# Kernel tuning notes

Measured on AMD Instinct MI355X. Metric: run time of the kernel, lower is better.

The kernel has to match this reference:

```python
import jax, jax.numpy as jnp
import numpy as np

IGNORE_T = 0.6
L_NOOBJ = 0.5
L_PRIOR = 0.01
L_COORD = 5.0
L_OBJ = 1.0
L_CLS = 1.0
PRIOR_EPOCHS = 12
EPS = 1e-8


def _iou_xyxy(a, b):
    # a, b: (..., 4) broadcastable xyxy boxes -> (...,) IoU
    ix1 = jnp.maximum(a[..., 0], b[..., 0])
    iy1 = jnp.maximum(a[..., 1], b[..., 1])
    ix2 = jnp.minimum(a[..., 2], b[..., 2])
    iy2 = jnp.minimum(a[..., 3], b[..., 3])
    inter = jnp.clip(ix2 - ix1, 0.0) * jnp.clip(iy2 - iy1, 0.0)
    area_a = jnp.clip(a[..., 2] - a[..., 0], 0.0) * jnp.clip(a[..., 3] - a[..., 1], 0.0)
    area_b = jnp.clip(b[..., 2] - b[..., 0], 0.0) * jnp.clip(b[..., 3] - b[..., 1], 0.0)
    return inter / (area_a + area_b - inter + EPS)


def setup_inputs() -> dict:
    key = jax.random.key(0)
    k1, k2, k3 = jax.random.split(key, 3)
    bs, G, A, C = 16, 19, 5, 20
    pred_tensor = jax.random.normal(k1, (bs, G, G, A, 5 + C), dtype=jnp.float32)
    gt_tensor = jax.random.uniform(k2, (bs, G, G, A, 5 + C), dtype=jnp.float32)
    anchors = jax.random.uniform(k3, (A, 2), dtype=jnp.float32)  # anchors_rel in (0,1)
    return {"pred_tensor": pred_tensor, "gt_tensor": gt_tensor, "anchors": anchors, "epoch": 5}


def reference(pred_tensor, gt_tensor, anchors, epoch):
    bs, G, _, A, _ = pred_tensor.shape
    f32 = pred_tensor.dtype
    px, py, pw, ph = (pred_tensor[..., i] for i in range(4))  # each [bs,G,G,A]
    po = pred_tensor[..., 4]
    pcls = pred_tensor[..., 5:]
    gx, gy, gw, gh = (gt_tensor[..., i] for i in range(4))
    go = gt_tensor[..., 4]
    gcls = gt_tensor[..., 5:]

    aw = anchors[:, 0].reshape(1, 1, 1, A)
    ah = anchors[:, 1].reshape(1, 1, 1, A)

    # YOLOv2 parameterization
    pbx, pby = jax.nn.sigmoid(px), jax.nn.sigmoid(py)
    pbw, pbh = jnp.exp(pw) * aw, jnp.exp(ph) * ah
    gbw, gbh = jnp.exp(gw) * aw, jnp.exp(gh) * ah

    ii = jnp.arange(G, dtype=f32).reshape(1, G, 1, 1)  # row index (y offset)
    jj = jnp.arange(G, dtype=f32).reshape(1, 1, G, 1)  # col index (x offset)

    def xywh2xyxy(x, y, w, h):
        cx, cy = x + jj, y + ii
        cw, ch = w * G, h * G
        return jnp.stack([cx - cw / 2, cy - ch / 2, cx + cw / 2, cy + ch / 2], axis=-1)

    pred_box = xywh2xyxy(pbx, pby, pbw, pbh)  # [bs,G,G,A,4]
    gt_box = xywh2xyxy(gx, gy, gbw, gbh)      # [bs,G,G,A,4]

    # part 1: max IoU of each prediction vs all positive gts (densified, masked)
    N = G * G * A
    pf = pred_box.reshape(bs, N, 4)
    gf = gt_box.reshape(bs, N, 4)
    gmask = (go > 0.5).reshape(bs, N).astype(f32)
    iou = _iou_xyxy(pf[:, :, None, :], gf[:, None, :, :])  # [bs,N,N]
    # IoU >= 0, so multiplying by the mask and taking max matches the torch
    # per-image nonzero-gather loop (and yields 0 when an image has no gt).
    max_iou = jnp.max(iou * gmask[:, None, :], axis=2).reshape(bs, G, G, A)

    noobj_mask = ((go <= 0.5) & (max_iou < IGNORE_T)).astype(f32)
    pconf = jax.nn.sigmoid(po)
    loss_noobj = L_NOOBJ * noobj_mask * pconf ** 2

    # part 2: prior (anchor-fitting) loss for early epochs
    pred_xywh = pred_tensor[..., 0:4]
    if epoch < PRIOR_EPOCHS:
        loss_prior = (L_PRIOR * pred_xywh ** 2).sum()
    else:
        loss_prior = jnp.zeros((), dtype=f32)

    # part 3: positive-sample losses
    pos = (go > 0.5).astype(f32)  # [bs,G,G,A]
    fitt_xywh = jnp.stack([jax.nn.sigmoid(px), jax.nn.sigmoid(py), pw, ph], axis=-1)
    gt_xywh = gt_tensor[..., 0:4]
    loss_xywh = L_COORD * pos[..., None] * (gt_xywh - fitt_xywh) ** 2

    conf_iou = _iou_xyxy(pred_box, gt_box)  # [bs,G,G,A]
    loss_conf = L_OBJ * pos * (conf_iou - jax.lax.stop_gradient(pconf)) ** 2

    pprob = jax.nn.softmax(pcls, axis=-1)
    loss_cls = L_CLS * pos[..., None] * (gcls - pprob) ** 2

    total = (loss_noobj.sum() + loss_prior + loss_xywh.sum()
             + loss_conf.sum() + loss_cls.sum()) / bs
    return total
```

## Files before the change

### kernel.cpp

```cpp
#include <hip/hip_runtime.h>

#define G_ 19
#define A_ 5
#define C_ 20
#define BS_ 16
#define N_ (G_*G_*A_)
#define CHK 8
#define SEG 256
#define NBLK (BS_*CHK)
#define EPSF 1e-8f

#define OFF_P1  0
#define OFF_CP  (OFF_P1 + NBLK*4)
#define OFF_CN  (OFF_CP + NBLK*4)
#define OFF_PLB (OFF_CN + NBLK*4 + 4)
#define OFF_PLA (OFF_PLB + NBLK*SEG*16)
#define OFF_NLB (OFF_PLA + NBLK*SEG*4)
#define OFF_NLV (OFF_NLB + NBLK*SEG*16)
#define OFF_FLG (OFF_NLV + NBLK*SEG*4)

__device__ __forceinline__ float sigmoidf_(float x) {
    return 1.0f / (1.0f + __expf(-x));
}

__global__ __launch_bounds__(256) void k1_elemwise(
    const float* __restrict__ pred, const float* __restrict__ gt,
    const float* __restrict__ anch, const int* __restrict__ epoch_p,
    char* __restrict__ ws, float* __restrict__ out)
{
    float*    partial1 = (float*)(ws + OFF_P1);
    unsigned* cntP  = (unsigned*)(ws + OFF_CP);
    unsigned* cntN  = (unsigned*)(ws + OFF_CN);
    float4*   plbox = (float4*)(ws + OFF_PLB);
    float*    plab  = (float*) (ws + OFF_PLA);
    float4*   nlbox = (float4*)(ws + OFF_NLB);
    float*    nlval = (float*) (ws + OFF_NLV);
    unsigned* flags = (unsigned*)(ws + OFF_FLG);

    __shared__ __align__(16) float sp[256*25];
    __shared__ __align__(16) float sg[256*25];
    __shared__ float red[4];
    __shared__ int wpo[4], wno[4];

    const int tid  = threadIdx.x;
    const int lane = tid & 63, wid = tid >> 6;
    const int b    = blockIdx.y;
    const int ch   = blockIdx.x;
    const int blin = b * CHK + ch;

    flags[blin*SEG + tid] = 0u;
    if (blin == 0 && tid == 0) out[0] = 0.f;

    int n0   = ch * 256;
    int rows = min(256, N_ - n0);
    int ndw  = rows * 25;
    const float* srcP = pred + ((size_t)b*N_ + n0)*25;
    const float* srcG = gt   + ((size_t)b*N_ + n0)*25;
    for (int d = tid; d < ndw; d += 256) { sp[d] = srcP[d]; sg[d] = srcG[d]; }
    __syncthreads();

    int n = n0 + tid;
    bool valid = tid < rows;
    const float* P = sp + tid*25;
    const float* T = sg + tid*25;
    float local = 0.f;

    bool pos = false;
    float gx1=0, gy1=0, gx2=0, gy2=0, area_g=0;
    float px1=0, py1=0, px2=0, py2=0, pconf=0;

    if (valid) {
        int a  = n % A_;
        int g2 = (n / A_) % G_;
        int g1 = n / (A_ * G_);
        float px = P[0], py = P[1], pw = P[2], ph = P[3], po = P[4];
        float gx = T[0], gy = T[1], gw = T[2], gh = T[3], go = T[4];
        float aw = anch[a*2+0], ah = anch[a*2+1];

        float sx  = sigmoidf_(px), sy = sigmoidf_(py);
        float pbw = __expf(pw) * aw, pbh = __expf(ph) * ah;
        float gbw = __expf(gw) * aw, gbh = __expf(gh) * ah;

        float cxp = sx + (float)g2, cyp = sy + (float)g1;
        float hwp = pbw * (0.5f * G_), hhp = pbh * (0.5f * G_);
        px1 = cxp - hwp; py1 = cyp - hhp; px2 = cxp + hwp; py2 = cyp + hhp;

        float cxg = gx + (float)g2, cyg = gy + (float)g1;
        float hwg = gbw * (0.5f * G_), hhg = gbh * (0.5f * G_);
        gx1 = cxg - hwg; gy1 = cyg - hhg; gx2 = cxg + hwg; gy2 = cyg + hhg;

        pconf = sigmoidf_(po);
        float area_p = fmaxf(px2 - px1, 0.f) * fmaxf(py2 - py1, 0.f);
        area_g = fmaxf(gx2 - gx1, 0.f) * fmaxf(gy2 - gy1, 0.f);

        if (*epoch_p < 12) {
            local += 0.01f * (px*px + py*py + pw*pw + ph*ph);
        }
        pos = go > 0.5f;
        if (pos) {
            float d0 = gx - sx, d1 = gy - sy, d2 = gw - pw, d3 = gh - ph;
            local += 5.0f * (d0*d0 + d1*d1 + d2*d2 + d3*d3);
            float ix1 = fmaxf(px1, gx1), iy1 = fmaxf(py1, gy1);
            float ix2 = fminf(px2, gx2), iy2 = fminf(py2, gy2);
            float iw = fmaxf(ix2 - ix1, 0.f), ih = fmaxf(iy2 - iy1, 0.f);
            float inter = iw * ih;
            float iou = inter / (area_p + area_g - inter + EPSF);
            float dc = iou - pconf;
            local += dc * dc;
            float cl[C_];
            float m = -1e30f;
            #pragma unroll
            for (int c = 0; c < C_; c++) { cl[c] = P[5+c]; m = fmaxf(m, cl[c]); }
            float s = 0.f;
            #pragma unroll
            for (int c = 0; c < C_; c++) { cl[c] = __expf(cl[c] - m); s += cl[c]; }
            float inv = 1.0f / s;
            float acc = 0.f;
            #pragma unroll
            for (int c = 0; c < C_; c++) { float d = T[5+c] - cl[c]*inv; acc += d*d; }
            local += acc;
        }
        local *= (1.0f / BS_);
    }

    bool isPos = valid && pos;
    bool isNeg = valid && !pos;
    unsigned long long mp = __ballot(isPos);
    unsigned long long mn = __ballot(isNeg);
    unsigned long long ltm = (1ull << lane) - 1ull;
    int ppre = __popcll(mp & ltm);
    int npre = __popcll(mn & ltm);
    if (lane == 0) { wpo[wid] = __popcll(mp); wno[wid] = __popcll(mn); }
    __syncthreads();
    int pexc = 0, nexc = 0, tp = 0, tn = 0;
    #pragma unroll
    for (int w = 0; w < 4; w++) {
        if (w < wid) { pexc += wpo[w]; nexc += wno[w]; }
        tp += wpo[w]; tn += wno[w];
    }
    if (isPos) {
        int k = blin*SEG + pexc + ppre;
        plbox[k] = make_float4(gx1, gy1, gx2, gy2);
        plab[k]  = area_g;
    } else if (isNeg) {
        int k = blin*SEG + nexc + npre;
        nlbox[k] = make_float4(px1, py1, px2, py2);
        nlval[k] = (0.5f / BS_) * pconf * pconf;
    }
    if (tid == 0) { cntP[blin] = (unsigned)tp; cntN[blin] = (unsigned)tn; }

    for (int off = 32; off; off >>= 1) local += __shfl_down(local, off);
    if (lane == 0) red[wid] = local;
    __syncthreads();
    if (tid == 0) partial1[blin] = red[0] + red[1] + red[2] + red[3];
}

__global__ __launch_bounds__(256) void k2_pairmax(char* __restrict__ ws)
{
    const unsigned* cntP  = (const unsigned*)(ws + OFF_CP);
    const unsigned* cntN  = (const unsigned*)(ws + OFF_CN);
    const float4*   plbox = (const float4*)(ws + OFF_PLB);
    const float*    plab  = (const float*) (ws + OFF_PLA);
    const float4*   nlbox = (const float4*)(ws + OFF_NLB);
    unsigned*       flags = (unsigned*)(ws + OFF_FLG);

    const int jc = blockIdx.x;
    const int ip = blockIdx.y;
    const int b  = blockIdx.z;
    const int tid = threadIdx.x;

    const int jblin = b*CHK + jc;
    const int iblin0 = b*CHK + ip*2;
    const int iblin1 = iblin0 + 1;

    int jlen = (int)cntP[jblin];
    if (jlen <= 0) return;

    __shared__ float4 sbox[SEG];
    __shared__ float  sb06[SEG];
    if (tid < jlen) {
        sbox[tid] = plbox[jblin*SEG + tid];
        sb06[tid] = -0.6f * plab[jblin*SEG + tid];
    }
    __syncthreads();

    int n0 = (int)cntN[iblin0], n1 = (int)cntN[iblin1];
    bool v0 = tid < n0, v1 = tid < n1;
    float4 p0 = v0 ? nlbox[iblin0*SEG + tid] : make_float4(0,0,0,0);
    float4 p1 = v1 ? nlbox[iblin1*SEG + tid] : make_float4(0,0,0,0);
    float c0 = (p0.z - p0.x) * (p0.w - p0.y) + EPSF;
    float c1 = (p1.z - p1.x) * (p1.w - p1.y) + EPSF;

    float md0 = -1e30f, md1 = -1e30f;
    for (int j = 0; j < jlen; j++) {
        float4 g = sbox[j];
        float tt = sb06[j];
        float ax0 = fmaxf(p0.x, g.x), ay0 = fmaxf(p0.y, g.y);
        float bx0 = fminf(p0.z, g.z), by0 = fminf(p0.w, g.w);
        float in0 = fmaxf(bx0 - ax0, 0.f) * fmaxf(by0 - ay0, 0.f);
        md0 = fmaxf(md0, fmaf(1.6f, in0, tt));
        float ax1 = fmaxf(p1.x, g.x), ay1 = fmaxf(p1.y, g.y);
        float bx1 = fminf(p1.z, g.z), by1 = fminf(p1.w, g.w);
        float in1 = fmaxf(bx1 - ax1, 0.f) * fmaxf(by1 - ay1, 0.f);
        md1 = fmaxf(md1, fmaf(1.6f, in1, tt));
    }
    if (v0 && md0 >= 0.6f * c0) flags[iblin0*SEG + tid] = 1u;
    if (v1 && md1 >= 0.6f * c1) flags[iblin1*SEG + tid] = 1u;
}

__global__ __launch_bounds__(256) void k3_final(char* __restrict__ ws,
                                                float* __restrict__ out)
{
    const float*    partial1 = (const float*)(ws + OFF_P1);
    const unsigned* cntN  = (const unsigned*)(ws + OFF_CN);
    const float*    nlval = (const float*) (ws + OFF_NLV);
    const unsigned* flags = (const unsigned*)(ws + OFF_FLG);

    const int tid  = threadIdx.x;
    const int blin = blockIdx.x;
    const int lane = tid & 63, wid = tid >> 6;

    float v = 0.f;
    if (tid < (int)cntN[blin] && flags[blin*SEG + tid] == 0u)
        v = nlval[blin*SEG + tid];
    if (tid == 0) v += partial1[blin];

    for (int off = 32; off; off >>= 1) v += __shfl_down(v, off);
    __shared__ float red[4];
    if (lane == 0) red[wid] = v;
    __syncthreads();
    if (tid == 0) atomicAdd(out, red[0] + red[1] + red[2] + red[3]);
}

extern "C" void kernel_launch(void* const* d_in, const int* in_sizes, int n_in,
                              void* d_out, int out_size, void* d_ws, size_t ws_size,
                              hipStream_t stream) {
    const float* pred  = (const float*)d_in[0];
    const float* gt_   = (const float*)d_in[1];
    const float* anch  = (const float*)d_in[2];
    const int*   epoch = (const int*)d_in[3];
    float* out = (float*)d_out;
    char*  ws  = (char*)d_ws;

    dim3 g1(CHK, BS_);
    k1_elemwise<<<g1, 256, 0, stream>>>(pred, gt_, anch, epoch, ws, out);
    dim3 g2(CHK, CHK/2, BS_);
    k2_pairmax<<<g2, 256, 0, stream>>>(ws);
    k3_final<<<NBLK, 256, 0, stream>>>(ws, out);
}
```

Before: 28.50 us.

## Fuse pair-max and final reduction via per-image ticket and bitmask

Merges the pairwise max-IoU kernel and the final reduction kernel into one launch. Per-image ignore flags become 64-bit ballot masks combined with atomicOr, and the last-arriving block for each image, found through an atomic ticket counter, performs the masked sum of the no-object terms. The load of full chunks into shared memory is unrolled, and the -0.6 area scaling moves into the first kernel. This removes one kernel launch and the flag array traffic, at the cost of atomics, thread fences and a serialized tail reduction per image.

```diff
diff --git a/kernel.cpp b/kernel.cpp
--- a/kernel.cpp
+++ b/kernel.cpp
@@ -13,11 +13,12 @@
 #define OFF_P1  0
 #define OFF_CP  (OFF_P1 + NBLK*4)
 #define OFF_CN  (OFF_CP + NBLK*4)
-#define OFF_PLB (OFF_CN + NBLK*4 + 4)
+#define OFF_TK  (OFF_CN + NBLK*4)
+#define OFF_MSK (OFF_TK + 64)
+#define OFF_PLB (OFF_MSK + BS_*32*8)
 #define OFF_PLA (OFF_PLB + NBLK*SEG*16)
 #define OFF_NLB (OFF_PLA + NBLK*SEG*4)
 #define OFF_NLV (OFF_NLB + NBLK*SEG*16)
-#define OFF_FLG (OFF_NLV + NBLK*SEG*4)
 
 __device__ __forceinline__ float sigmoidf_(float x) {
     return 1.0f / (1.0f + __expf(-x));
@@ -31,11 +32,12 @@
     float*    partial1 = (float*)(ws + OFF_P1);
     unsigned* cntP  = (unsigned*)(ws + OFF_CP);
     unsigned* cntN  = (unsigned*)(ws + OFF_CN);
+    unsigned* ticket = (unsigned*)(ws + OFF_TK);
+    unsigned long long* mask = (unsigned long long*)(ws + OFF_MSK);
     float4*   plbox = (float4*)(ws + OFF_PLB);
     float*    plab  = (float*) (ws + OFF_PLA);
     float4*   nlbox = (float4*)(ws + OFF_NLB);
     float*    nlval = (float*) (ws + OFF_NLV);
-    unsigned* flags = (unsigned*)(ws + OFF_FLG);
 
     __shared__ __align__(16) float sp[256*25];
     __shared__ __align__(16) float sg[256*25];
@@ -48,15 +50,23 @@
     const int ch   = blockIdx.x;
     const int blin = b * CHK + ch;
 
-    flags[blin*SEG + tid] = 0u;
+    if (tid < 4)               mask[blin*4 + tid] = 0ull;
+    if (ch == 0 && tid == 0)   ticket[b] = 0u;
     if (blin == 0 && tid == 0) out[0] = 0.f;
 
     int n0   = ch * 256;
     int rows = min(256, N_ - n0);
-    int ndw  = rows * 25;
     const float* srcP = pred + ((size_t)b*N_ + n0)*25;
     const float* srcG = gt   + ((size_t)b*N_ + n0)*25;
-    for (int d = tid; d < ndw; d += 256) { sp[d] = srcP[d]; sg[d] = srcG[d]; }
+    if (rows == 256) {
+        #pragma unroll
+        for (int k = 0; k < 25; k++) sp[tid + k*256] = srcP[tid + k*256];
+        #pragma unroll
+        for (int k = 0; k < 25; k++) sg[tid + k*256] = srcG[tid + k*256];
+    } else {
+        int ndw = rows * 25;
+        for (int d = tid; d < ndw; d += 256) { sp[d] = srcP[d]; sg[d] = srcG[d]; }
+    }
     __syncthreads();
 
     int n = n0 + tid;
@@ -141,7 +151,7 @@
     if (isPos) {
         int k = blin*SEG + pexc + ppre;
         plbox[k] = make_float4(gx1, gy1, gx2, gy2);
-        plab[k]  = area_g;
+        plab[k]  = -0.6f * area_g;
     } else if (isNeg) {
         int k = blin*SEG + nexc + npre;
         nlbox[k] = make_float4(px1, py1, px2, py2);
@@ -155,78 +165,96 @@
     if (tid == 0) partial1[blin] = red[0] + red[1] + red[2] + red[3];
 }
 
-__global__ __launch_bounds__(256) void k2_pairmax(char* __restrict__ ws)
+__global__ __launch_bounds__(256) void k2_fused(char* __restrict__ ws,
+                                                float* __restrict__ out)
 {
+    const float*    partial1 = (const float*)(ws + OFF_P1);
     const unsigned* cntP  = (const unsigned*)(ws + OFF_CP);
     const unsigned* cntN  = (const unsigned*)(ws + OFF_CN);
+    unsigned*       ticket = (unsigned*)(ws + OFF_TK);
+    unsigned long long* mask = (unsigned long long*)(ws + OFF_MSK);
     const float4*   plbox = (const float4*)(ws + OFF_PLB);
     const float*    plab  = (const float*) (ws + OFF_PLA);
     const float4*   nlbox = (const float4*)(ws + OFF_NLB);
-    unsigned*       flags = (unsigned*)(ws + OFF_FLG);
-
+    const float*    nlval = (const float*) (ws + OFF_NLV);
+
+    const int tid = threadIdx.x;
+    const int lane = tid & 63, wid = tid >> 6;
     const int jc = blockIdx.x;
     const int ip = blockIdx.y;
     const int b  = blockIdx.z;
-    const int tid = threadIdx.x;
-
-    const int jblin = b*CHK + jc;
+
+    const int jblin  = b*CHK + jc;
     const int iblin0 = b*CHK + ip*2;
     const int iblin1 = iblin0 + 1;
 
-    int jlen = (int)cntP[jblin];
-    if (jlen <= 0) return;
-
     __shared__ float4 sbox[SEG];
     __shared__ float  sb06[SEG];
+    __shared__ int    sFin;
+    __shared__ unsigned long long smask[32];
+    __shared__ float  red[4];
+
+    const int jlen = (int)cntP[jblin];
     if (tid < jlen) {
         sbox[tid] = plbox[jblin*SEG + tid];
-        sb06[tid] = -0.6f * plab[jblin*SEG + tid];
-    }
-    __syncthreads();
-
-    int n0 = (int)cntN[iblin0], n1 = (int)cntN[iblin1];
-    bool v0 = tid < n0, v1 = tid < n1;
-    float4 p0 = v0 ? nlbox[iblin0*SEG + tid] : make_float4(0,0,0,0);
-    float4 p1 = v1 ? nlbox[iblin1*SEG + tid] : make_float4(0,0,0,0);
-    float c0 = (p0.z - p0.x) * (p0.w - p0.y) + EPSF;
-    float c1 = (p1.z - p1.x) * (p1.w - p1.y) + EPSF;
-
-    float md0 = -1e30f, md1 = -1e30f;
-    for (int j = 0; j < jlen; j++) {
-        float4 g = sbox[j];
-        float tt = sb06[j];
-        float ax0 = fmaxf(p0.x, g.x), ay0 = fmaxf(p0.y, g.y);
-        float bx0 = fminf(p0.z, g.z), by0 = fminf(p0.w, g.w);
-        float in0 = fmaxf(bx0 - ax0, 0.f) * fmaxf(by0 - ay0, 0.f);
-        md0 = fmaxf(md0, fmaf(1.6f, in0, tt));
-        float ax1 = fmaxf(p1.x, g.x), ay1 = fmaxf(p1.y, g.y);
-        float bx1 = fminf(p1.z, g.z), by1 = fminf(p1.w, g.w);
-        float in1 = fmaxf(bx1 - ax1, 0.f) * fmaxf(by1 - ay1, 0.f);
-        md1 = fmaxf(md1, fmaf(1.6f, in1, tt));
-    }
-    if (v0 && md0 >= 0.6f * c0) flags[iblin0*SEG + tid] = 1u;
-    if (v1 && md1 >= 0.6f * c1) flags[iblin1*SEG + tid] = 1u;
-}
-
-__global__ __launch_bounds__(256) void k3_final(char* __restrict__ ws,
-                                                float* __restrict__ out)
-{
-    const float*    partial1 = (const float*)(ws + OFF_P1);
-    const unsigned* cntN  = (const unsigned*)(ws + OFF_CN);
-    const float*    nlval = (const float*) (ws + OFF_NLV);
-    const unsigned* flags = (const unsigned*)(ws + OFF_FLG);
-
-    const int tid  = threadIdx.x;
-    const int blin = blockIdx.x;
-    const int lane = tid & 63, wid = tid >> 6;
+        sb06[tid] = plab [jblin*SEG + tid];
+    }
+    __syncthreads();
+
+    if (jlen > 0) {
+        int n0 = (int)cntN[iblin0], n1 = (int)cntN[iblin1];
+        bool v0 = tid < n0, v1 = tid < n1;
+        float4 p0 = nlbox[iblin0*SEG + tid];
+        float4 p1 = nlbox[iblin1*SEG + tid];
+        float t00 = 0.6f * ((p0.z - p0.x) * (p0.w - p0.y) + EPSF);
+        float t01 = 0.6f * ((p1.z - p1.x) * (p1.w - p1.y) + EPSF);
+
+        float md0 = -3e38f, md1 = -3e38f;
+        #pragma unroll 2
+        for (int j = 0; j < jlen; j++) {
+            float4 g = sbox[j];
+            float a06 = sb06[j];
+            float ax0 = fmaxf(p0.x, g.x), ay0 = fmaxf(p0.y, g.y);
+            float bx0 = fminf(p0.z, g.z), by0 = fminf(p0.w, g.w);
+            float in0 = fmaxf(bx0 - ax0, 0.f) * fmaxf(by0 - ay0, 0.f);
+            md0 = fmaxf(md0, fmaf(1.6f, in0, a06));
+            float ax1 = fmaxf(p1.x, g.x), ay1 = fmaxf(p1.y, g.y);
+            float bx1 = fminf(p1.z, g.z), by1 = fminf(p1.w, g.w);
+            float in1 = fmaxf(bx1 - ax1, 0.f) * fmaxf(by1 - ay1, 0.f);
+            md1 = fmaxf(md1, fmaf(1.6f, in1, a06));
+        }
+        unsigned long long e0 = __ballot(v0 && md0 >= t00);
+        unsigned long long e1 = __ballot(v1 && md1 >= t01);
+        if (lane == 0) {
+            if (e0) atomicOr(&mask[b*32 + (ip*2  )*4 + wid], e0);
+            if (e1) atomicOr(&mask[b*32 + (ip*2+1)*4 + wid], e1);
+        }
+    }
+
+    __threadfence();
+    if (tid == 0) {
+        unsigned old = atomicAdd(&ticket[b], 1u);
+        sFin = (old == 31u);
+    }
+    __syncthreads();
+    if (!sFin) return;
+
+    __threadfence();
+    if (tid < 32) smask[tid] = atomicOr(&mask[b*32 + tid], 0ull);
+    __syncthreads();
 
     float v = 0.f;
-    if (tid < (int)cntN[blin] && flags[blin*SEG + tid] == 0u)
-        v = nlval[blin*SEG + tid];
-    if (tid == 0) v += partial1[blin];
+    #pragma unroll
+    for (int r = 0; r < 8; r++) {
+        int slot = r*256 + tid;
+        int k = slot & 255;
+        if (k < (int)cntN[b*CHK + (slot >> 8)] &&
+            !((smask[slot >> 6] >> (slot & 63)) & 1ull))
+            v += nlval[b*CHK*SEG + slot];
+    }
+    if (tid < CHK) v += partial1[b*CHK + tid];
 
     for (int off = 32; off; off >>= 1) v += __shfl_down(v, off);
-    __shared__ float red[4];
     if (lane == 0) red[wid] = v;
     __syncthreads();
     if (tid == 0) atomicAdd(out, red[0] + red[1] + red[2] + red[3]);
@@ -245,6 +273,5 @@
     dim3 g1(CHK, BS_);
     k1_elemwise<<<g1, 256, 0, stream>>>(pred, gt_, anch, epoch, ws, out);
     dim3 g2(CHK, CHK/2, BS_);
-    k2_pairmax<<<g2, 256, 0, stream>>>(ws);
-    k3_final<<<NBLK, 256, 0, stream>>>(ws, out);
-}
+    k2_fused<<<g2, 256, 0, stream>>>(ws, out);
+}
```

Result: slower. 55.25 us (+93.9%).

## Compact negative pairs per thread, pad positive lists, read gt boxes via uniform loads

Applied to the files above, without the earlier changes.

The pairwise max-IoU kernel now packs the negatives of two segments into one thread each instead of two per thread. It reads positive gt boxes straight from global memory through a wave-uniform base, which drops the shared-memory staging and its barrier. The positive lists are padded to a multiple of four with sentinel boxes so the inner loop can unroll by four, and the -0.6 area scale is precomputed in k1. The full-chunk input copy is also unrolled. The padding adds extra writes in k1, and fewer active threads per block lowers parallelism but removes redundant work when both segments are half-full.

```diff
diff --git a/kernel.cpp b/kernel.cpp
--- a/kernel.cpp
+++ b/kernel.cpp
@@ -53,10 +53,17 @@
 
     int n0   = ch * 256;
     int rows = min(256, N_ - n0);
-    int ndw  = rows * 25;
     const float* srcP = pred + ((size_t)b*N_ + n0)*25;
     const float* srcG = gt   + ((size_t)b*N_ + n0)*25;
-    for (int d = tid; d < ndw; d += 256) { sp[d] = srcP[d]; sg[d] = srcG[d]; }
+    if (rows == 256) {
+        #pragma unroll
+        for (int k = 0; k < 25; k++) sp[tid + k*256] = srcP[tid + k*256];
+        #pragma unroll
+        for (int k = 0; k < 25; k++) sg[tid + k*256] = srcG[tid + k*256];
+    } else {
+        int ndw = rows * 25;
+        for (int d = tid; d < ndw; d += 256) { sp[d] = srcP[d]; sg[d] = srcG[d]; }
+    }
     __syncthreads();
 
     int n = n0 + tid;
@@ -141,13 +148,18 @@
     if (isPos) {
         int k = blin*SEG + pexc + ppre;
         plbox[k] = make_float4(gx1, gy1, gx2, gy2);
-        plab[k]  = area_g;
+        plab[k]  = -0.6f * area_g;
     } else if (isNeg) {
         int k = blin*SEG + nexc + npre;
         nlbox[k] = make_float4(px1, py1, px2, py2);
         nlval[k] = (0.5f / BS_) * pconf * pconf;
     }
-    if (tid == 0) { cntP[blin] = (unsigned)tp; cntN[blin] = (unsigned)tn; }
+    int padTo = (tp + 3) & ~3;
+    if (tid >= tp && tid < padTo) {
+        plbox[blin*SEG + tid] = make_float4(3e8f, 3e8f, 3e8f, 3e8f);
+        plab [blin*SEG + tid] = -3e38f;
+    }
+    if (tid == 0) { cntP[blin] = (unsigned)padTo; cntN[blin] = (unsigned)tn; }
 
     for (int off = 32; off; off >>= 1) local += __shfl_down(local, off);
     if (lane == 0) red[wid] = local;
@@ -164,48 +176,43 @@
     const float4*   nlbox = (const float4*)(ws + OFF_NLB);
     unsigned*       flags = (unsigned*)(ws + OFF_FLG);
 
-    const int jc = blockIdx.x;
-    const int ip = blockIdx.y;
-    const int b  = blockIdx.z;
     const int tid = threadIdx.x;
-
-    const int jblin = b*CHK + jc;
+    const int jc  = blockIdx.x;
+    const int ip  = blockIdx.y;
+    const int b   = blockIdx.z;
+
+    const int jblin  = b*CHK + jc;
     const int iblin0 = b*CHK + ip*2;
     const int iblin1 = iblin0 + 1;
 
-    int jlen = (int)cntP[jblin];
+    const int jlen = (int)cntP[jblin];
     if (jlen <= 0) return;
 
-    __shared__ float4 sbox[SEG];
-    __shared__ float  sb06[SEG];
-    if (tid < jlen) {
-        sbox[tid] = plbox[jblin*SEG + tid];
-        sb06[tid] = -0.6f * plab[jblin*SEG + tid];
-    }
-    __syncthreads();
-
-    int n0 = (int)cntN[iblin0], n1 = (int)cntN[iblin1];
-    bool v0 = tid < n0, v1 = tid < n1;
-    float4 p0 = v0 ? nlbox[iblin0*SEG + tid] : make_float4(0,0,0,0);
-    float4 p1 = v1 ? nlbox[iblin1*SEG + tid] : make_float4(0,0,0,0);
-    float c0 = (p0.z - p0.x) * (p0.w - p0.y) + EPSF;
-    float c1 = (p1.z - p1.x) * (p1.w - p1.y) + EPSF;
-
-    float md0 = -1e30f, md1 = -1e30f;
-    for (int j = 0; j < jlen; j++) {
-        float4 g = sbox[j];
-        float tt = sb06[j];
-        float ax0 = fmaxf(p0.x, g.x), ay0 = fmaxf(p0.y, g.y);
-        float bx0 = fminf(p0.z, g.z), by0 = fminf(p0.w, g.w);
-        float in0 = fmaxf(bx0 - ax0, 0.f) * fmaxf(by0 - ay0, 0.f);
-        md0 = fmaxf(md0, fmaf(1.6f, in0, tt));
-        float ax1 = fmaxf(p1.x, g.x), ay1 = fmaxf(p1.y, g.y);
-        float bx1 = fminf(p1.z, g.z), by1 = fminf(p1.w, g.w);
-        float in1 = fmaxf(bx1 - ax1, 0.f) * fmaxf(by1 - ay1, 0.f);
-        md1 = fmaxf(md1, fmaf(1.6f, in1, tt));
-    }
-    if (v0 && md0 >= 0.6f * c0) flags[iblin0*SEG + tid] = 1u;
-    if (v1 && md1 >= 0.6f * c1) flags[iblin1*SEG + tid] = 1u;
+    const int tn0 = (int)cntN[iblin0];
+    const int tn1 = (int)cntN[iblin1];
+    const bool valid = tid < tn0 + tn1;
+    const int  seg  = (tid < tn0) ? iblin0 : iblin1;
+    const int  k    = (tid < tn0) ? tid : tid - tn0;
+    float4 p = nlbox[seg*SEG + min(k, 255)];
+    float t0 = 0.6f * ((p.z - p.x) * (p.w - p.y) + EPSF);
+
+    const int jbase = __builtin_amdgcn_readfirstlane(jblin * SEG);
+    const float4* jb = plbox + jbase;
+    const float*  ja = plab  + jbase;
+
+    float md = -3e38f;
+    for (int j = 0; j < jlen; j += 4) {
+        #pragma unroll
+        for (int t = 0; t < 4; t++) {
+            float4 g = jb[j + t];
+            float a06 = ja[j + t];
+            float ax = fmaxf(p.x, g.x), ay = fmaxf(p.y, g.y);
+            float bx = fminf(p.z, g.z), by = fminf(p.w, g.w);
+            float in0 = fmaxf(bx - ax, 0.f) * fmaxf(by - ay, 0.f);
+            md = fmaxf(md, fmaf(1.6f, in0, a06));
+        }
+    }
+    if (valid && md >= t0) flags[seg*SEG + k] = 1u;
 }
 
 __global__ __launch_bounds__(256) void k3_final(char* __restrict__ ws,
```

Measured after the change: 25.31 us. 1.13x faster.
